# Optimization experiments

Measured on AMD Instinct MI355X. Metric: run time of the kernel, lower is better.

## Reference

```python
import jax, jax.numpy as jnp
import numpy as np
import math

ALPHA_MIN = math.exp(-1.0 / 5.0)   # ~0.8187
ALPHA_MAX = math.exp(-1.0 / 25.0)  # ~0.9608
THRESHOLD = 1.0


def setup_inputs() -> dict:
    key = jax.random.key(0)
    k1, k2, k3, k4, k5 = jax.random.split(key, 5)
    B, T, I, H = 32, 2048, 256, 512
    x = jax.random.normal(k1, (B, T, I), dtype=jnp.float32)
    # Linear weight, kaiming-ish scale
    W = jax.random.normal(k2, (H, I), dtype=jnp.float32) * (1.0 / np.sqrt(I))
    # alpha ~ U[exp(-1/5), exp(-1/25)] as in nn.init.uniform_
    alpha = ALPHA_MIN + jax.random.uniform(k3, (H,), dtype=jnp.float32) * (ALPHA_MAX - ALPHA_MIN)
    # initial membrane potential / spike state (torch.rand in _lif_cell)
    u0 = jax.random.uniform(k4, (B, H), dtype=jnp.float32)
    s0 = jax.random.uniform(k5, (B, H), dtype=jnp.float32)
    return {"x": x, "W": W, "alpha": alpha, "u0": u0, "s0": s0}


def reference(x, W, alpha, u0, s0):
    # clamp alpha to its admissible range (lif_feature has no 'NoClamp')
    alpha = jnp.clip(alpha, ALPHA_MIN, ALPHA_MAX)
    b = 1.0 - alpha  # lif_feature has no 'B'

    # feedforward projection: [B, T, H]
    Wx = jnp.einsum('bti,hi->bth', x, W)

    def step(carry, wx_t):
        ut, st = carry
        ut = alpha * (ut - st) + b * wx_t          # leaky integrate + soft reset
        st = (ut - THRESHOLD > 0).astype(ut.dtype)  # heaviside spike
        return (ut, st), st

    # scan over time: Wx -> [T, B, H]
    _, s = jax.lax.scan(step, (u0, s0), jnp.swapaxes(Wx, 0, 1))
    return jnp.swapaxes(s, 0, 1)  # [B, T, H]
```

## Files before the change

### kernel.cpp

```cpp
#include <hip/hip_runtime.h>

#define ALPHA_MIN 0.8187307530779818f
#define ALPHA_MAX 0.9607894391523232f

typedef _Float16 f16;
typedef _Float16 f16x8 __attribute__((ext_vector_type(8)));
typedef float f32x16 __attribute__((ext_vector_type(16)));

#define BB_ 32
#define TT_ 2048
#define KK_ 256
#define HH_ 512
#define TC_ 64
#define NC_ (TT_ / TC_)
#define NB_ 64

__global__ __launch_bounds__(320, 2) void lif_fused(
    const float* __restrict__ X,
    const float* __restrict__ W,
    const float* __restrict__ alpha,
    const float* __restrict__ u0,
    const float* __restrict__ s0,
    float* __restrict__ out)
{
    __shared__ float wxbuf[2][TC_ * NB_];

    const int b  = blockIdx.x & 31;
    const int nt = blockIdx.x >> 5;
    const int n0 = nt * NB_;

    const int tid  = threadIdx.x;
    const int wv   = tid >> 6;
    const int lane = tid & 63;
    const int fm   = lane & 31;
    const int fq   = lane >> 5;

    if (wv < 4) {
        const int mh = wv >> 1;
        const int nh = wv & 1;
        const int ncol = n0 + nh * 32 + fm;

        f16x8 bh[16], bl[16];
        {
            const float* wp = W + (size_t)ncol * KK_ + fq * 8;
#pragma unroll
            for (int ks = 0; ks < 16; ++ks) {
                float4 v0 = *(const float4*)(wp + ks * 16);
                float4 v1 = *(const float4*)(wp + ks * 16 + 4);
                float v[8] = {v0.x, v0.y, v0.z, v0.w, v1.x, v1.y, v1.z, v1.w};
                f16x8 h, l;
#pragma unroll
                for (int j = 0; j < 8; ++j) {
                    const f16 hj = (f16)v[j];
                    h[j] = hj;
                    l[j] = (f16)((v[j] - (float)hj) * 2048.0f);
                }
                bh[ks] = h; bl[ks] = l;
            }
        }

        f32x16 accH, accL;
#pragma unroll
        for (int e = 0; e < 16; ++e) { accH[e] = 0.0f; accL[e] = 0.0f; }

        const float* xrow = X + ((size_t)b * TT_ + mh * 32 + fm) * KK_ + fq * 8;

        float4 abuf[4][2];
        auto pref = [&](int ki) {
            if (ki < NC_ * 16) {
                const float* p = xrow + (size_t)(ki >> 4) * (TC_ * KK_) + (ki & 15) * 16;
                abuf[ki & 3][0] = *(const float4*)p;
                abuf[ki & 3][1] = *(const float4*)(p + 4);
            }
        };
        pref(0); pref(1); pref(2); pref(3);

        for (int c = 0; c < NC_; ++c) {
            int ki = c * 16;
#pragma unroll
            for (int ks = 0; ks < 16; ++ks, ++ki) {
                const float4 a0 = abuf[ki & 3][0];
                const float4 a1 = abuf[ki & 3][1];
                pref(ki + 4);
                const float v[8] = {a0.x, a0.y, a0.z, a0.w, a1.x, a1.y, a1.z, a1.w};
                f16x8 ah, al;
#pragma unroll
                for (int j = 0; j < 8; ++j) {
                    const f16 hj = (f16)v[j];
                    ah[j] = hj;
                    al[j] = (f16)((v[j] - (float)hj) * 2048.0f);
                }
                accH = __builtin_amdgcn_mfma_f32_32x32x16_f16(ah, bh[ks], accH, 0, 0, 0);
                accL = __builtin_amdgcn_mfma_f32_32x32x16_f16(ah, bl[ks], accL, 0, 0, 0);
                accL = __builtin_amdgcn_mfma_f32_32x32x16_f16(al, bh[ks], accL, 0, 0, 0);
            }
            float* wb = &wxbuf[c & 1][0];
#pragma unroll
            for (int r = 0; r < 16; ++r) {
                const int row = mh * 32 + (r & 3) + 8 * (r >> 2) + 4 * fq;
                wb[row * NB_ + nh * 32 + fm] = accH[r] + accL[r] * (1.0f / 2048.0f);
                accH[r] = 0.0f; accL[r] = 0.0f;
            }
            __syncthreads();
        }
    } else {
        const int h = n0 + lane;
        const int chain = b * HH_ + h;
        float a = alpha[h];
        a = fminf(fmaxf(a, ALPHA_MIN), ALPHA_MAX);
        const float bbv = 1.0f - a;
        float u = u0[chain];
        float s = s0[chain];
        float* op = out + (size_t)b * TT_ * HH_ + h;

        for (int c = 0; c < NC_; ++c) {
            if (c > 0) {
                const float* wb = &wxbuf[(c - 1) & 1][0];
                const int tbase = (c - 1) * TC_;
                for (int t0 = 0; t0 < TC_; t0 += 8) {
                    float w[8];
#pragma unroll
                    for (int j = 0; j < 8; ++j) w[j] = wb[(t0 + j) * NB_ + lane];
#pragma unroll
                    for (int j = 0; j < 8; ++j) {
                        u = fmaf(a, u - s, bbv * w[j]);
                        s = (u > 1.0f) ? 1.0f : 0.0f;
                        __builtin_nontemporal_store(s, &op[(size_t)(tbase + t0 + j) * HH_]);
                    }
                }
            }
            __syncthreads();
        }
        {
            const float* wb = &wxbuf[(NC_ - 1) & 1][0];
            const int tbase = (NC_ - 1) * TC_;
            for (int t0 = 0; t0 < TC_; t0 += 8) {
                float w[8];
#pragma unroll
                for (int j = 0; j < 8; ++j) w[j] = wb[(t0 + j) * NB_ + lane];
#pragma unroll
                for (int j = 0; j < 8; ++j) {
                    u = fmaf(a, u - s, bbv * w[j]);
                    s = (u > 1.0f) ? 1.0f : 0.0f;
                    __builtin_nontemporal_store(s, &op[(size_t)(tbase + t0 + j) * HH_]);
                }
            }
        }
    }
}

__global__ void gemm_naive(const float* __restrict__ X, const float* __restrict__ W,
                           float* __restrict__ C, int M, int N, int K)
{
    const int idx = blockIdx.x * 256 + threadIdx.x;
    if (idx >= M * N) return;
    const int m = idx / N, n = idx % N;
    float acc = 0.0f;
    for (int k = 0; k < K; ++k) acc = fmaf(X[(size_t)m * K + k], W[(size_t)n * K + k], acc);
    C[idx] = acc;
}

__global__ __launch_bounds__(64) void lif_scan_inplace(
    float* __restrict__ buf, const float* __restrict__ alpha,
    const float* __restrict__ u0, const float* __restrict__ s0, int T, int H)
{
    const int chain = blockIdx.x * 64 + threadIdx.x;
    const int h = chain % H;
    const int b = chain / H;
    float a = alpha[h];
    a = fminf(fmaxf(a, ALPHA_MIN), ALPHA_MAX);
    const float bb = 1.0f - a;
    float u = u0[chain], s = s0[chain];
    float* base = buf + (size_t)b * T * H + h;
    for (int t = 0; t < T; ++t) {
        u = fmaf(a, u - s, bb * base[(size_t)t * H]);
        s = (u > 1.0f) ? 1.0f : 0.0f;
        base[(size_t)t * H] = s;
    }
}

extern "C" void kernel_launch(void* const* d_in, const int* in_sizes, int n_in,
                              void* d_out, int out_size, void* d_ws, size_t ws_size,
                              hipStream_t stream) {
    const float* x     = (const float*)d_in[0];
    const float* W     = (const float*)d_in[1];
    const float* alpha = (const float*)d_in[2];
    const float* u0    = (const float*)d_in[3];
    const float* s0    = (const float*)d_in[4];
    float* out = (float*)d_out;

    const int H = in_sizes[2];
    const int I = in_sizes[1] / H;
    const int B = in_sizes[3] / H;
    const int T = in_sizes[0] / (B * I);

    if (B == BB_ && T == TT_ && I == KK_ && H == HH_) {
        lif_fused<<<256, 320, 0, stream>>>(x, W, alpha, u0, s0, out);
    } else {
        const int M = B * T;
        gemm_naive<<<(M * H + 255) / 256, 256, 0, stream>>>(x, W, out, M, H, I);
        lif_scan_inplace<<<(B * H + 63) / 64, 64, 0, stream>>>(out, alpha, u0, s0, T, H);
    }
}
```

Measured before the change: 321.7 us.

## Double producer waves to compute two time chunks per sync in fused LIF kernel

After: 382.2 us. 1.19x slower.

```diff
diff --git a/kernel.cpp b/kernel.cpp
--- a/kernel.cpp
+++ b/kernel.cpp
@@ -12,10 +12,10 @@
 #define KK_ 256
 #define HH_ 512
 #define TC_ 64
-#define NC_ (TT_ / TC_)
+#define NSC 16
 #define NB_ 64
 
-__global__ __launch_bounds__(320, 2) void lif_fused(
+__global__ __launch_bounds__(576, 2) void lif_fused2(
     const float* __restrict__ X,
     const float* __restrict__ W,
     const float* __restrict__ alpha,
@@ -23,7 +23,7 @@
     const float* __restrict__ s0,
     float* __restrict__ out)
 {
-    __shared__ float wxbuf[2][TC_ * NB_];
+    __shared__ float wxbuf[4][TC_ * NB_];
 
     const int b  = blockIdx.x & 31;
     const int nt = blockIdx.x >> 5;
@@ -35,8 +35,9 @@
     const int fm   = lane & 31;
     const int fq   = lane >> 5;
 
-    if (wv < 4) {
-        const int mh = wv >> 1;
+    if (wv < 8) {
+        const int g  = wv >> 2;
+        const int mh = (wv >> 1) & 1;
         const int nh = wv & 1;
         const int ncol = n0 + nh * 32 + fm;
 
@@ -63,25 +64,26 @@
 #pragma unroll
         for (int e = 0; e < 16; ++e) { accH[e] = 0.0f; accL[e] = 0.0f; }
 
-        const float* xrow = X + ((size_t)b * TT_ + mh * 32 + fm) * KK_ + fq * 8;
+        const float* xrow = X + ((size_t)b * TT_ + g * TC_ + mh * 32 + fm) * KK_ + fq * 8;
 
-        float4 abuf[4][2];
+        float4 abuf[8][2];
         auto pref = [&](int ki) {
-            if (ki < NC_ * 16) {
-                const float* p = xrow + (size_t)(ki >> 4) * (TC_ * KK_) + (ki & 15) * 16;
-                abuf[ki & 3][0] = *(const float4*)p;
-                abuf[ki & 3][1] = *(const float4*)(p + 4);
+            if (ki < NSC * 16) {
+                const float* p = xrow + (size_t)(ki >> 4) * (2 * TC_ * KK_) + (ki & 15) * 16;
+                abuf[ki & 7][0] = *(const float4*)p;
+                abuf[ki & 7][1] = *(const float4*)(p + 4);
             }
         };
-        pref(0); pref(1); pref(2); pref(3);
+#pragma unroll
+        for (int i = 0; i < 8; ++i) pref(i);
 
-        for (int c = 0; c < NC_; ++c) {
-            int ki = c * 16;
+        for (int sc = 0; sc < NSC; ++sc) {
+            int ki = sc * 16;
 #pragma unroll
             for (int ks = 0; ks < 16; ++ks, ++ki) {
-                const float4 a0 = abuf[ki & 3][0];
-                const float4 a1 = abuf[ki & 3][1];
-                pref(ki + 4);
+                const float4 a0 = abuf[ki & 7][0];
+                const float4 a1 = abuf[ki & 7][1];
+                pref(ki + 8);
                 const float v[8] = {a0.x, a0.y, a0.z, a0.w, a1.x, a1.y, a1.z, a1.w};
                 f16x8 ah, al;
 #pragma unroll
@@ -94,7 +96,7 @@
                 accL = __builtin_amdgcn_mfma_f32_32x32x16_f16(ah, bl[ks], accL, 0, 0, 0);
                 accL = __builtin_amdgcn_mfma_f32_32x32x16_f16(al, bh[ks], accL, 0, 0, 0);
             }
-            float* wb = &wxbuf[c & 1][0];
+            float* wb = &wxbuf[(sc & 1) * 2 + g][0];
 #pragma unroll
             for (int r = 0; r < 16; ++r) {
                 const int row = mh * 32 + (r & 3) + 8 * (r >> 2) + 4 * fq;
@@ -113,10 +115,11 @@
         float s = s0[chain];
         float* op = out + (size_t)b * TT_ * HH_ + h;
 
-        for (int c = 0; c < NC_; ++c) {
-            if (c > 0) {
-                const float* wb = &wxbuf[(c - 1) & 1][0];
-                const int tbase = (c - 1) * TC_;
+        auto consume_pair = [&](int p) {
+#pragma unroll
+            for (int half = 0; half < 2; ++half) {
+                const float* wb = &wxbuf[(p & 1) * 2 + half][0];
+                const int tbase = (2 * p + half) * TC_;
                 for (int t0 = 0; t0 < TC_; t0 += 8) {
                     float w[8];
 #pragma unroll
@@ -129,23 +132,13 @@
                     }
                 }
             }
+        };
+
+        for (int sc = 0; sc < NSC; ++sc) {
+            if (sc > 0) consume_pair(sc - 1);
             __syncthreads();
         }
-        {
-            const float* wb = &wxbuf[(NC_ - 1) & 1][0];
-            const int tbase = (NC_ - 1) * TC_;
-            for (int t0 = 0; t0 < TC_; t0 += 8) {
-                float w[8];
-#pragma unroll
-                for (int j = 0; j < 8; ++j) w[j] = wb[(t0 + j) * NB_ + lane];
-#pragma unroll
-                for (int j = 0; j < 8; ++j) {
-                    u = fmaf(a, u - s, bbv * w[j]);
-                    s = (u > 1.0f) ? 1.0f : 0.0f;
-                    __builtin_nontemporal_store(s, &op[(size_t)(tbase + t0 + j) * HH_]);
-                }
-            }
-        }
+        consume_pair(NSC - 1);
     }
 }
 
@@ -195,7 +188,7 @@
     const int T = in_sizes[0] / (B * I);
 
     if (B == BB_ && T == TT_ && I == KK_ && H == HH_) {
-        lif_fused<<<256, 320, 0, stream>>>(x, W, alpha, u0, s0, out);
+        lif_fused2<<<256, 576, 0, stream>>>(x, W, alpha, u0, s0, out);
     } else {
         const int M = B * T;
         gemm_naive<<<(M * H + 255) / 256, 256, 0, stream>>>(x, W, out, M, H, I);
```

## Stage fp16 split of X tiles in shared memory with swizzled layout

Applied to the files above, without the earlier changes.

New measurement: 280.6 us. 12.8% less time.

```diff
diff --git a/kernel.cpp b/kernel.cpp
--- a/kernel.cpp
+++ b/kernel.cpp
@@ -4,6 +4,7 @@
 #define ALPHA_MAX 0.9607894391523232f
 
 typedef _Float16 f16;
+typedef _Float16 f16x4 __attribute__((ext_vector_type(4)));
 typedef _Float16 f16x8 __attribute__((ext_vector_type(8)));
 typedef float f32x16 __attribute__((ext_vector_type(16)));
 
@@ -12,10 +13,15 @@
 #define KK_ 256
 #define HH_ 512
 #define TC_ 64
-#define NC_ (TT_ / TC_)
-#define NB_ 64
-
-__global__ __launch_bounds__(320, 2) void lif_fused(
+#define NC_ 32
+#define KH_ 128
+
+__device__ __forceinline__ void barrier_lds() {
+    __builtin_amdgcn_s_waitcnt(0xC07F);
+    __builtin_amdgcn_s_barrier();
+}
+
+__global__ __launch_bounds__(320, 1) void lif_fused4(
     const float* __restrict__ X,
     const float* __restrict__ W,
     const float* __restrict__ alpha,
@@ -23,11 +29,13 @@
     const float* __restrict__ s0,
     float* __restrict__ out)
 {
-    __shared__ float wxbuf[2][TC_ * NB_];
+    __shared__ f16 Ah[TC_ * KH_];
+    __shared__ f16 Al[TC_ * KH_];
+    __shared__ float wxbuf[2][TC_ * 64];
 
     const int b  = blockIdx.x & 31;
     const int nt = blockIdx.x >> 5;
-    const int n0 = nt * NB_;
+    const int n0 = nt * 64;
 
     const int tid  = threadIdx.x;
     const int wv   = tid >> 6;
@@ -38,11 +46,10 @@
     if (wv < 4) {
         const int mh = wv >> 1;
         const int nh = wv & 1;
-        const int ncol = n0 + nh * 32 + fm;
 
         f16x8 bh[16], bl[16];
         {
-            const float* wp = W + (size_t)ncol * KK_ + fq * 8;
+            const float* wp = W + (size_t)(n0 + nh * 32 + fm) * KK_ + fq * 8;
 #pragma unroll
             for (int ks = 0; ks < 16; ++ks) {
                 float4 v0 = *(const float4*)(wp + ks * 16);
@@ -59,49 +66,77 @@
             }
         }
 
-        f32x16 accH, accL;
-#pragma unroll
-        for (int e = 0; e < 16; ++e) { accH[e] = 0.0f; accL[e] = 0.0f; }
-
-        const float* xrow = X + ((size_t)b * TT_ + mh * 32 + fm) * KK_ + fq * 8;
-
-        float4 abuf[4][2];
-        auto pref = [&](int ki) {
-            if (ki < NC_ * 16) {
-                const float* p = xrow + (size_t)(ki >> 4) * (TC_ * KK_) + (ki & 15) * 16;
-                abuf[ki & 3][0] = *(const float4*)p;
-                abuf[ki & 3][1] = *(const float4*)(p + 4);
-            }
-        };
-        pref(0); pref(1); pref(2); pref(3);
+        f32x16 accH, accLa, accLb;
+#pragma unroll
+        for (int e = 0; e < 16; ++e) { accH[e] = 0.0f; accLa[e] = 0.0f; accLb[e] = 0.0f; }
+
+        const int srow_j = wv * 16 + (lane >> 5);
+        const int f4i    = lane & 31;
+        const int g      = f4i >> 1;
+        const int sub    = f4i & 1;
+
+        float4 pend[8];
+        auto issue_loads = [&](int c, int kh) {
+            const float* base = X + ((size_t)b * TT_ + c * TC_) * KK_ + kh * KH_ + f4i * 4;
+#pragma unroll
+            for (int j = 0; j < 8; ++j)
+                pend[j] = *(const float4*)(base + (size_t)(srow_j + j * 2) * KK_);
+        };
+        auto cvt_write = [&]() {
+#pragma unroll
+            for (int j = 0; j < 8; ++j) {
+                const int row = srow_j + j * 2;
+                const float v[4] = {pend[j].x, pend[j].y, pend[j].z, pend[j].w};
+                f16x4 h, l;
+#pragma unroll
+                for (int e = 0; e < 4; ++e) {
+                    const f16 he = (f16)v[e];
+                    h[e] = he;
+                    l[e] = (f16)((v[e] - (float)he) * 2048.0f);
+                }
+                const int addr = row * KH_ + ((g ^ (row & 15)) * 8) + sub * 4;
+                *(f16x4*)&Ah[addr] = h;
+                *(f16x4*)&Al[addr] = l;
+            }
+        };
+        auto compute_half = [&](int hf) {
+            const int row = mh * 32 + fm;
+            const int r15 = row & 15;
+#pragma unroll
+            for (int ks = 0; ks < 8; ++ks) {
+                const int addr = row * KH_ + (((ks * 2 + fq) ^ r15) * 8);
+                const f16x8 ah = *(const f16x8*)&Ah[addr];
+                const f16x8 al = *(const f16x8*)&Al[addr];
+                const int ksg = hf * 8 + ks;
+                accH  = __builtin_amdgcn_mfma_f32_32x32x16_f16(ah, bh[ksg], accH,  0, 0, 0);
+                accLa = __builtin_amdgcn_mfma_f32_32x32x16_f16(ah, bl[ksg], accLa, 0, 0, 0);
+                accLb = __builtin_amdgcn_mfma_f32_32x32x16_f16(al, bh[ksg], accLb, 0, 0, 0);
+            }
+        };
+
+        issue_loads(0, 0);
 
         for (int c = 0; c < NC_; ++c) {
-            int ki = c * 16;
-#pragma unroll
-            for (int ks = 0; ks < 16; ++ks, ++ki) {
-                const float4 a0 = abuf[ki & 3][0];
-                const float4 a1 = abuf[ki & 3][1];
-                pref(ki + 4);
-                const float v[8] = {a0.x, a0.y, a0.z, a0.w, a1.x, a1.y, a1.z, a1.w};
-                f16x8 ah, al;
-#pragma unroll
-                for (int j = 0; j < 8; ++j) {
-                    const f16 hj = (f16)v[j];
-                    ah[j] = hj;
-                    al[j] = (f16)((v[j] - (float)hj) * 2048.0f);
-                }
-                accH = __builtin_amdgcn_mfma_f32_32x32x16_f16(ah, bh[ks], accH, 0, 0, 0);
-                accL = __builtin_amdgcn_mfma_f32_32x32x16_f16(ah, bl[ks], accL, 0, 0, 0);
-                accL = __builtin_amdgcn_mfma_f32_32x32x16_f16(al, bh[ks], accL, 0, 0, 0);
-            }
-            float* wb = &wxbuf[c & 1][0];
-#pragma unroll
-            for (int r = 0; r < 16; ++r) {
-                const int row = mh * 32 + (r & 3) + 8 * (r >> 2) + 4 * fq;
-                wb[row * NB_ + nh * 32 + fm] = accH[r] + accL[r] * (1.0f / 2048.0f);
-                accH[r] = 0.0f; accL[r] = 0.0f;
-            }
-            __syncthreads();
+            cvt_write();
+            issue_loads(c, 1);
+            barrier_lds();
+            compute_half(0);
+            barrier_lds();
+            cvt_write();
+            if (c + 1 < NC_) issue_loads(c + 1, 0);
+            barrier_lds();
+            compute_half(1);
+            {
+                float* wb = &wxbuf[c & 1][0];
+                const int colw = nh * 32 + fm;
+#pragma unroll
+                for (int r = 0; r < 16; ++r) {
+                    const int roww = mh * 32 + (r & 3) + 8 * (r >> 2) + 4 * fq;
+                    wb[roww * 64 + colw] = accH[r] + (accLa[r] + accLb[r]) * (1.0f / 2048.0f);
+                    accH[r] = 0.0f; accLa[r] = 0.0f; accLb[r] = 0.0f;
+                }
+            }
+            barrier_lds();
         }
     } else {
         const int h = n0 + lane;
@@ -113,39 +148,33 @@
         float s = s0[chain];
         float* op = out + (size_t)b * TT_ * HH_ + h;
 
-        for (int c = 0; c < NC_; ++c) {
-            if (c > 0) {
-                const float* wb = &wxbuf[(c - 1) & 1][0];
-                const int tbase = (c - 1) * TC_;
-                for (int t0 = 0; t0 < TC_; t0 += 8) {
-                    float w[8];
-#pragma unroll
-                    for (int j = 0; j < 8; ++j) w[j] = wb[(t0 + j) * NB_ + lane];
-#pragma unroll
-                    for (int j = 0; j < 8; ++j) {
-                        u = fmaf(a, u - s, bbv * w[j]);
-                        s = (u > 1.0f) ? 1.0f : 0.0f;
-                        __builtin_nontemporal_store(s, &op[(size_t)(tbase + t0 + j) * HH_]);
-                    }
-                }
-            }
-            __syncthreads();
-        }
-        {
-            const float* wb = &wxbuf[(NC_ - 1) & 1][0];
-            const int tbase = (NC_ - 1) * TC_;
-            for (int t0 = 0; t0 < TC_; t0 += 8) {
+        auto consume = [&](int c, int hf) {
+            const float* wb = &wxbuf[c & 1][0];
+            const int tb = c * TC_ + hf * 32;
+#pragma unroll
+            for (int t0 = 0; t0 < 32; t0 += 8) {
                 float w[8];
 #pragma unroll
-                for (int j = 0; j < 8; ++j) w[j] = wb[(t0 + j) * NB_ + lane];
+                for (int j = 0; j < 8; ++j) w[j] = wb[(hf * 32 + t0 + j) * 64 + lane];
 #pragma unroll
                 for (int j = 0; j < 8; ++j) {
                     u = fmaf(a, u - s, bbv * w[j]);
                     s = (u > 1.0f) ? 1.0f : 0.0f;
-                    __builtin_nontemporal_store(s, &op[(size_t)(tbase + t0 + j) * HH_]);
-                }
-            }
+                    __builtin_nontemporal_store(s, &op[(size_t)(tb + t0 + j) * HH_]);
+                }
+            }
+        };
+
+        for (int c = 0; c < NC_; ++c) {
+            barrier_lds();
+            if (c > 0) consume(c - 1, 0);
+            barrier_lds();
+            barrier_lds();
+            if (c > 0) consume(c - 1, 1);
+            barrier_lds();
         }
+        consume(NC_ - 1, 0);
+        consume(NC_ - 1, 1);
     }
 }
 
@@ -195,7 +224,7 @@
     const int T = in_sizes[0] / (B * I);
 
     if (B == BB_ && T == TT_ && I == KK_ && H == HH_) {
-        lif_fused<<<256, 320, 0, stream>>>(x, W, alpha, u0, s0, out);
+        lif_fused4<<<256, 320, 0, stream>>>(x, W, alpha, u0, s0, out);
     } else {
         const int M = B * T;
         gemm_naive<<<(M * H + 255) / 256, 256, 0, stream>>>(x, W, out, M, H, I);
```
